# Optimization experiments

Measured on AMD Instinct MI355X. Metric: run time of the kernel, lower is better.

The kernel has to match this reference:

```python
import jax, jax.numpy as jnp
import numpy as np

N = 100_000
E = 1_600_000
H = 128
L = 3
EPS = 1e-5


def setup_inputs() -> dict:
    key = jax.random.key(0)
    ks = jax.random.split(key, 8)
    x = jax.random.normal(ks[0], (N, H), dtype=jnp.float32)
    edge_index = jax.random.randint(ks[1], (2, E), 0, N, dtype=jnp.int64)
    edge_weight = jax.random.uniform(ks[2], (E,), dtype=jnp.float32)
    # per-layer params (all layers are H->H since in_dim == hidden)
    s = 1.0 / np.sqrt(H)
    lin_neigh_w = jax.random.uniform(ks[3], (L, H, H), minval=-s, maxval=s, dtype=jnp.float32)
    lin_root_w = jax.random.uniform(ks[4], (L, H, H), minval=-s, maxval=s, dtype=jnp.float32)
    lin_root_b = jax.random.uniform(ks[5], (L, H), minval=-s, maxval=s, dtype=jnp.float32)
    ln_w = jnp.ones((L, H), dtype=jnp.float32)
    ln_b = jnp.zeros((L, H), dtype=jnp.float32)
    return {"x": x, "edge_index": edge_index, "edge_weight": edge_weight,
            "lin_neigh_w": lin_neigh_w, "lin_root_w": lin_root_w,
            "lin_root_b": lin_root_b, "ln_w": ln_w, "ln_b": ln_b}


def _layer(h, src, dst, e_w, w_neigh, w_root, b_root, g, b):
    # message: m_ij = w_ij * x_j ; aggregate: scatter-add over dst, normalized by sum of weights
    msg = e_w[:, None] * h[src]                                    # [E, H]
    agg = jax.ops.segment_sum(msg, dst, num_segments=N)            # [N, H]
    sum_w = jnp.clip(jax.ops.segment_sum(e_w, dst, num_segments=N), 1.0, None)
    out = agg / sum_w[:, None]
    out = out @ w_neigh.T + h @ w_root.T + b_root                  # lin_neigh + lin_root
    out = jax.nn.relu(out)
    # per-node LayerNorm over feature dim
    mu = jnp.mean(out, axis=-1, keepdims=True)
    var = jnp.var(out, axis=-1, keepdims=True)
    out = (out - mu) * jax.lax.rsqrt(var + EPS) * g + b
    return out  # dropout: inference no-op


def reference(x, edge_index, edge_weight, lin_neigh_w, lin_root_w, lin_root_b, ln_w, ln_b):
    src, dst = edge_index[0], edge_index[1]
    h = x
    for l in range(L):
        h = _layer(h, src, dst, edge_weight, lin_neigh_w[l], lin_root_w[l],
                   lin_root_b[l], ln_w[l], ln_b[l])
    return h
```

## Files before the change

kernel.cpp:

```cpp
#include <hip/hip_runtime.h>
#include <hip/hip_fp16.h>

#define H 128
#define EPS 1e-5f
#define BCAP 6144

typedef __attribute__((ext_vector_type(8))) _Float16 half8;
typedef __attribute__((ext_vector_type(4))) float f32x4;

__device__ inline __half2 u2h2(unsigned u) { return __builtin_bit_cast(__half2, u); }
__device__ inline unsigned h22u(__half2 h) { return __builtin_bit_cast(unsigned, h); }

__global__ void convert_kernel(const float* __restrict__ x, unsigned* __restrict__ hx, int n4) {
    int i = blockIdx.x * 256 + threadIdx.x;
    if (i >= n4) return;
    float4 v = reinterpret_cast<const float4*>(x)[i];
    unsigned p0 = h22u(__floats2half2_rn(v.x, v.y));
    unsigned p1 = h22u(__floats2half2_rn(v.z, v.w));
    reinterpret_cast<uint2*>(hx)[i] = make_uint2(p0, p1);
}

__global__ __launch_bounds__(256) void bhist_kernel(const int* __restrict__ dst,
                                                    int* __restrict__ ghist, int E, int NB) {
    __shared__ int hist[512];
    int t = threadIdx.x;
    for (int i = t; i < NB; i += 256) hist[i] = 0;
    __syncthreads();
    int base = blockIdx.x * 8192 + t;
#pragma unroll
    for (int k = 0; k < 32; ++k) {
        int e = base + k * 256;
        if (e < E) atomicAdd(&hist[dst[e] >> 8], 1);
    }
    __syncthreads();
    for (int i = t; i < NB; i += 256)
        if (hist[i]) atomicAdd(&ghist[i], hist[i]);
}

__global__ __launch_bounds__(512) void bscan_kernel(const int* __restrict__ ghist,
                                                    int* __restrict__ bucket_base,
                                                    int* __restrict__ cursor,
                                                    int* __restrict__ row_start,
                                                    int NB, int E, int N) {
    __shared__ int lds[512];
    int t = threadIdx.x;
    int v = (t < NB) ? ghist[t] : 0;
    lds[t] = v;
    __syncthreads();
    for (int off = 1; off < 512; off <<= 1) {
        int u = (t >= off) ? lds[t - off] : 0;
        __syncthreads();
        lds[t] += u;
        __syncthreads();
    }
    int excl = lds[t] - v;
    if (t < NB) {
        bucket_base[t] = excl;
        cursor[t] = excl;
    }
    if (t == 0) {
        bucket_base[NB] = E;
        row_start[N] = E;
    }
}

__global__ __launch_bounds__(1024) void bucketize_kernel(const int* __restrict__ src,
                                                         const int* __restrict__ dst,
                                                         const float* __restrict__ ew,
                                                         int* __restrict__ cursor,
                                                         int2* __restrict__ ee, int E, int NB) {
    __shared__ int hist[512];
    __shared__ int scn[512];
    __shared__ int gbase[512];
    __shared__ int2 stage[8192];
    int t = threadIdx.x;
    for (int i = t; i < NB; i += 1024) hist[i] = 0;
    __syncthreads();

    int e0 = blockIdx.x * 8192;
    int bb[8], rk[8], pk[8], wb[8];
#pragma unroll
    for (int k = 0; k < 8; ++k) {
        int e = e0 + t + k * 1024;
        if (e < E) {
            int s = src[e], d = dst[e];
            bb[k] = d >> 8;
            pk[k] = s | ((d & 255) << 17);
            wb[k] = __float_as_int(ew[e]);
            rk[k] = atomicAdd(&hist[bb[k]], 1);
        } else {
            bb[k] = -1;
        }
    }
    __syncthreads();
    if (t < 512) scn[t] = (t < NB) ? hist[t] : 0;
    __syncthreads();
    for (int off = 1; off < 512; off <<= 1) {
        int u = 0;
        if (t < 512 && t >= off) u = scn[t - off];
        __syncthreads();
        if (t < 512) scn[t] += u;
        __syncthreads();
    }
    for (int i = t; i < NB; i += 1024) {
        int c = hist[i];
        if (c > 0) gbase[i] = atomicAdd(&cursor[i], c);
    }
#pragma unroll
    for (int k = 0; k < 8; ++k) {
        if (bb[k] >= 0) {
            int start = scn[bb[k]] - hist[bb[k]];
            stage[start + rk[k]] = make_int2(pk[k], wb[k]);
        }
    }
    __syncthreads();
    int wv = t >> 6, ln = t & 63;
    for (int bk = wv; bk < NB; bk += 16) {
        int c = hist[bk];
        if (c == 0) continue;
        int s0 = scn[bk] - c;
        int gb = gbase[bk];
        for (int i = ln; i < c; i += 64) ee[gb + i] = stage[s0 + i];
    }
}

__global__ __launch_bounds__(256) void bsort_kernel(int2* __restrict__ ee,
                                                    const int* __restrict__ bucket_base,
                                                    int* __restrict__ row_start, int N) {
    __shared__ int cnts[256];
    __shared__ int scv[256];
    __shared__ int prefs[256];
    __shared__ int2 out[BCAP];
    int b = blockIdx.x;
    int base = bucket_base[b], endb = bucket_base[b + 1];
    int cnt = endb - base;
    int t = threadIdx.x;
    cnts[t] = 0;
    __syncthreads();
    for (int i = base + t; i < endb; i += 256) atomicAdd(&cnts[(ee[i].x >> 17) & 255], 1);
    __syncthreads();
    scv[t] = cnts[t];
    __syncthreads();
    for (int off = 1; off < 256; off <<= 1) {
        int u = (t >= off) ? scv[t - off] : 0;
        __syncthreads();
        scv[t] += u;
        __syncthreads();
    }
    int pref = scv[t] - cnts[t];
    prefs[t] = pref;
    int node = (b << 8) + t;
    if (node < N) row_start[node] = base + pref;
    __syncthreads();
    cnts[t] = 0;
    __syncthreads();
    for (int i = base + t; i < endb; i += 256) {
        int2 r = ee[i];
        int dl = (r.x >> 17) & 255;
        int rkk = atomicAdd(&cnts[dl], 1);
        int slot = prefs[dl] + rkk;
        if (slot < BCAP) out[slot] = make_int2(r.x & 0x1FFFF, r.y);
    }
    __syncthreads();
    {
        int s0 = prefs[t], c = cnts[t];
        float sw = 0.f;
        for (int k = 0; k < c; ++k) sw += __int_as_float(out[s0 + k].y);
        sw = sw < 1.f ? 1.f : sw;
        float inv = 1.f / sw;
        for (int k = 0; k < c; ++k) {
            float w = __int_as_float(out[s0 + k].y) * inv;
            unsigned hb = (unsigned)__half_as_ushort(__float2half(w));
            out[s0 + k].y = (int)(hb | (hb << 16));
        }
    }
    __syncthreads();
    for (int i = t; i < cnt; i += 256) ee[base + i] = out[i];
}

__global__ __launch_bounds__(256) void agg_kernel(const unsigned short* __restrict__ hx,
                                                  const int* __restrict__ row_start,
                                                  const int2* __restrict__ ee,
                                                  unsigned short* __restrict__ aggb, int N) {
    int t = threadIdx.x;
    int node = blockIdx.x * 4 + (t >> 6);
    if (node >= N) return;
    int lane = t & 63, half = lane >> 5, jb = lane & 31;
    __half2 a01 = u2h2(0), a23 = u2h2(0);
    int rs = row_start[node], re = row_start[node + 1];
    int i = rs + half;
    for (; i + 6 < re; i += 8) {
        int2 e0 = ee[i], e1 = ee[i + 2], e2 = ee[i + 4], e3 = ee[i + 6];
        uint2 u0 = reinterpret_cast<const uint2*>(hx + (size_t)e0.x * H)[jb];
        uint2 u1 = reinterpret_cast<const uint2*>(hx + (size_t)e1.x * H)[jb];
        uint2 u2 = reinterpret_cast<const uint2*>(hx + (size_t)e2.x * H)[jb];
        uint2 u3 = reinterpret_cast<const uint2*>(hx + (size_t)e3.x * H)[jb];
        __half2 w0 = u2h2((unsigned)e0.y), w1 = u2h2((unsigned)e1.y);
        __half2 w2 = u2h2((unsigned)e2.y), w3 = u2h2((unsigned)e3.y);
        a01 = __hfma2(u2h2(u0.x), w0, a01); a23 = __hfma2(u2h2(u0.y), w0, a23);
        a01 = __hfma2(u2h2(u1.x), w1, a01); a23 = __hfma2(u2h2(u1.y), w1, a23);
        a01 = __hfma2(u2h2(u2.x), w2, a01); a23 = __hfma2(u2h2(u2.y), w2, a23);
        a01 = __hfma2(u2h2(u3.x), w3, a01); a23 = __hfma2(u2h2(u3.y), w3, a23);
    }
    for (; i < re; i += 2) {
        int2 e0 = ee[i];
        uint2 u0 = reinterpret_cast<const uint2*>(hx + (size_t)e0.x * H)[jb];
        __half2 w0 = u2h2((unsigned)e0.y);
        a01 = __hfma2(u2h2(u0.x), w0, a01);
        a23 = __hfma2(u2h2(u0.y), w0, a23);
    }
    a01 = __hadd2(a01, u2h2((unsigned)__shfl_xor((int)h22u(a01), 32)));
    a23 = __hadd2(a23, u2h2((unsigned)__shfl_xor((int)h22u(a23), 32)));
    unsigned p = half ? h22u(a23) : h22u(a01);
    reinterpret_cast<unsigned*>(aggb + (size_t)node * H)[2 * jb + half] = p;
}

__global__ __launch_bounds__(256, 2) void gemm_ln_mfma(
    const unsigned short* __restrict__ aggb, const unsigned short* __restrict__ hx,
    const float* __restrict__ Wn, const float* __restrict__ Wr,
    const float* __restrict__ br, const float* __restrict__ g,
    const float* __restrict__ b, unsigned short* __restrict__ hout,
    float* __restrict__ outf, int final_layer, int N) {
    __shared__ half8 Bfl[4096];

    int t = threadIdx.x;
    int w = t >> 6, lane = t & 63;
    int Mbase = blockIdx.x * 256;

#pragma unroll
    for (int it = 0; it < 16; ++it) {
        int f = it * 4 + w;
        int kt = f >> 3, nb = f & 7;
        int n = nb * 16 + (lane & 15);
        int kk = (kt & 3) * 32 + (lane >> 4) * 8;
        const float* wp = ((kt < 4) ? Wn : Wr) + (size_t)n * H + kk;
        float4 wa = *reinterpret_cast<const float4*>(wp);
        float4 wb = *reinterpret_cast<const float4*>(wp + 4);
        half8 sv;
        sv[0] = (_Float16)wa.x; sv[1] = (_Float16)wa.y;
        sv[2] = (_Float16)wa.z; sv[3] = (_Float16)wa.w;
        sv[4] = (_Float16)wb.x; sv[5] = (_Float16)wb.y;
        sv[6] = (_Float16)wb.z; sv[7] = (_Float16)wb.w;
        Bfl[f * 64 + lane] = sv;
    }
    __syncthreads();

    int lrow = lane & 15, lk = lane >> 4;
    const char* aggp = (const char*)aggb;
    const char* hp = (const char*)hx;
    size_t rb[4];
#pragma unroll
    for (int mf = 0; mf < 4; ++mf) {
        int r = Mbase + w * 64 + mf * 16 + lrow;
        r = r < N ? r : N - 1;
        rb[mf] = (size_t)r * 256;
    }

    f32x4 acc[4][8];
#pragma unroll
    for (int mf = 0; mf < 4; ++mf)
#pragma unroll
        for (int nb = 0; nb < 8; ++nb) acc[mf][nb] = (f32x4){0.f, 0.f, 0.f, 0.f};

#pragma unroll
    for (int kt = 0; kt < 8; ++kt) {
        const char* base = (kt < 4) ? aggp : hp;
        int off = (kt & 3) * 64 + lk * 16;
        half8 bf[8];
#pragma unroll
        for (int nb = 0; nb < 8; ++nb) bf[nb] = Bfl[(kt * 8 + nb) * 64 + lane];
#pragma unroll
        for (int mf = 0; mf < 4; ++mf) {
            half8 av = *reinterpret_cast<const half8*>(base + rb[mf] + off);
#pragma unroll
            for (int nb = 0; nb < 8; ++nb)
                acc[mf][nb] = __builtin_amdgcn_mfma_f32_16x16x32_f16(av, bf[nb], acc[mf][nb], 0, 0, 0);
        }
    }

    int col0 = lane & 15, rq = lane >> 4;
    float bias[8], gg[8], bbv[8];
#pragma unroll
    for (int nb = 0; nb < 8; ++nb) {
        int c = col0 + nb * 16;
        bias[nb] = br[c];
        gg[nb] = g[c];
        bbv[nb] = b[c];
    }
#pragma unroll
    for (int mf = 0; mf < 4; ++mf) {
#pragma unroll
        for (int reg = 0; reg < 4; ++reg) {
            float v[8];
            float s = 0.f, q = 0.f;
#pragma unroll
            for (int nb = 0; nb < 8; ++nb) {
                float u = acc[mf][nb][reg] + bias[nb];
                u = fmaxf(u, 0.f);
                v[nb] = u;
                s += u;
                q = fmaf(u, u, q);
            }
#pragma unroll
            for (int off = 1; off < 16; off <<= 1) {
                s += __shfl_xor(s, off);
                q += __shfl_xor(q, off);
            }
            float mu = s * (1.f / 128.f);
            float var = q * (1.f / 128.f) - mu * mu;
            float inv = rsqrtf(var + EPS);
            int grow = Mbase + w * 64 + mf * 16 + rq * 4 + reg;
            if (grow < N) {
                if (final_layer) {
#pragma unroll
                    for (int nb = 0; nb < 8; ++nb)
                        outf[(size_t)grow * H + col0 + nb * 16] = (v[nb] - mu) * inv * gg[nb] + bbv[nb];
                } else {
#pragma unroll
                    for (int nb = 0; nb < 8; ++nb)
                        hout[(size_t)grow * H + col0 + nb * 16] =
                            __half_as_ushort(__float2half((v[nb] - mu) * inv * gg[nb] + bbv[nb]));
                }
            }
        }
    }
}

static inline size_t alignup(size_t x) { return (x + 255) & ~(size_t)255; }

extern "C" void kernel_launch(void* const* d_in, const int* in_sizes, int n_in,
                              void* d_out, int out_size, void* d_ws, size_t ws_size,
                              hipStream_t stream) {
    const float* x  = (const float*)d_in[0];
    const int*   ei = (const int*)d_in[1];
    const float* ew = (const float*)d_in[2];
    const float* Wn = (const float*)d_in[3];
    const float* Wr = (const float*)d_in[4];
    const float* br = (const float*)d_in[5];
    const float* g  = (const float*)d_in[6];
    const float* bb = (const float*)d_in[7];
    float* out = (float*)d_out;

    int N = in_sizes[0] / H;
    int E = in_sizes[2];
    const int* src = ei;
    const int* dst = ei + E;
    int NB = (N + 255) >> 8;

    char* ws = (char*)d_ws;
    size_t off = 0;
    int* ghist = (int*)(ws + off);         off = alignup(off + sizeof(int) * 512);
    int* bucket_base = (int*)(ws + off);   off = alignup(off + sizeof(int) * 513);
    int* cursor = (int*)(ws + off);        off = alignup(off + sizeof(int) * 512);
    int* row_start = (int*)(ws + off);     off = alignup(off + sizeof(int) * ((size_t)N + 1));
    int2* ee = (int2*)(ws + off);          off = alignup(off + sizeof(int2) * (size_t)E);
    unsigned short* aggb = (unsigned short*)(ws + off); off = alignup(off + 2ull * N * H);
    unsigned short* hx = (unsigned short*)(ws + off);   off = alignup(off + 2ull * N * H);

    int eblocks = (E + 8191) / 8192;

    hipMemsetAsync(ghist, 0, sizeof(int) * 512, stream);
    bhist_kernel<<<eblocks, 256, 0, stream>>>(dst, ghist, E, NB);
    bscan_kernel<<<1, 512, 0, stream>>>(ghist, bucket_base, cursor, row_start, NB, E, N);
    bucketize_kernel<<<eblocks, 1024, 0, stream>>>(src, dst, ew, cursor, ee, E, NB);
    bsort_kernel<<<NB, 256, 0, stream>>>(ee, bucket_base, row_start, N);

    int n4 = N * H / 4;
    convert_kernel<<<(n4 + 255) / 256, 256, 0, stream>>>(x, (unsigned*)hx, n4);

    int gblocks = (N + 255) / 256;
    for (int l = 0; l < 3; ++l) {
        agg_kernel<<<(N + 3) / 4, 256, 0, stream>>>(hx, row_start, ee, aggb, N);
        gemm_ln_mfma<<<gblocks, 256, 0, stream>>>(
            aggb, hx,
            Wn + (size_t)l * H * H, Wr + (size_t)l * H * H, br + (size_t)l * H,
            g + (size_t)l * H, bb + (size_t)l * H,
            hx, out, (l == 2) ? 1 : 0, N);
    }
}
```

Baseline: 333.5 us.

## Slice node features into 16-wide column blocks and pack edges into 32-bit records

```diff
diff --git a/kernel.cpp b/kernel.cpp
--- a/kernel.cpp
+++ b/kernel.cpp
@@ -4,6 +4,7 @@
 #define H 128
 #define EPS 1e-5f
 #define BCAP 6144
+#define SLB 2048
 
 typedef __attribute__((ext_vector_type(8))) _Float16 half8;
 typedef __attribute__((ext_vector_type(4))) float f32x4;
@@ -11,13 +12,22 @@
 __device__ inline __half2 u2h2(unsigned u) { return __builtin_bit_cast(__half2, u); }
 __device__ inline unsigned h22u(__half2 h) { return __builtin_bit_cast(unsigned, h); }
 
-__global__ void convert_kernel(const float* __restrict__ x, unsigned* __restrict__ hx, int n4) {
-    int i = blockIdx.x * 256 + threadIdx.x;
-    if (i >= n4) return;
-    float4 v = reinterpret_cast<const float4*>(x)[i];
-    unsigned p0 = h22u(__floats2half2_rn(v.x, v.y));
-    unsigned p1 = h22u(__floats2half2_rn(v.z, v.w));
-    reinterpret_cast<uint2*>(hx)[i] = make_uint2(p0, p1);
+__global__ void convert_kernel(const float* __restrict__ x, char* __restrict__ hxs, int N) {
+    int tid = blockIdx.x * 256 + threadIdx.x;
+    int twoN = N * 2;
+    if (tid >= twoN * 8) return;
+    int s = tid / twoN;
+    int rem = tid - s * twoN;
+    int nd = rem >> 1, hh = rem & 1;
+    const float* xp = x + (size_t)nd * H + s * 16 + hh * 8;
+    float4 a = *reinterpret_cast<const float4*>(xp);
+    float4 b2 = *reinterpret_cast<const float4*>(xp + 4);
+    unsigned p0 = h22u(__floats2half2_rn(a.x, a.y));
+    unsigned p1 = h22u(__floats2half2_rn(a.z, a.w));
+    unsigned p2 = h22u(__floats2half2_rn(b2.x, b2.y));
+    unsigned p3 = h22u(__floats2half2_rn(b2.z, b2.w));
+    *reinterpret_cast<uint4*>(hxs + (((size_t)s * N + nd) << 5) + hh * 16) =
+        make_uint4(p0, p1, p2, p3);
 }
 
 __global__ __launch_bounds__(256) void bhist_kernel(const int* __restrict__ dst,
@@ -124,9 +134,10 @@
     }
 }
 
-__global__ __launch_bounds__(256) void bsort_kernel(int2* __restrict__ ee,
+__global__ __launch_bounds__(256) void bsort_kernel(const int2* __restrict__ ee,
                                                     const int* __restrict__ bucket_base,
-                                                    int* __restrict__ row_start, int N) {
+                                                    int* __restrict__ row_start,
+                                                    unsigned* __restrict__ ee4, int N) {
     __shared__ int cnts[256];
     __shared__ int scv[256];
     __shared__ int prefs[256];
@@ -170,53 +181,58 @@
         float inv = 1.f / sw;
         for (int k = 0; k < c; ++k) {
             float w = __int_as_float(out[s0 + k].y) * inv;
-            unsigned hb = (unsigned)__half_as_ushort(__float2half(w));
-            out[s0 + k].y = (int)(hb | (hb << 16));
-        }
-    }
-    __syncthreads();
-    for (int i = t; i < cnt; i += 256) ee[base + i] = out[i];
-}
-
-__global__ __launch_bounds__(256) void agg_kernel(const unsigned short* __restrict__ hx,
+            out[s0 + k].y = (int)(unsigned)__half_as_ushort(__float2half(w));
+        }
+    }
+    __syncthreads();
+    for (int i = t; i < cnt; i += 256)
+        ee4[base + i] = ((unsigned)out[i].x << 15) | ((unsigned)out[i].y >> 1);
+}
+
+__global__ __launch_bounds__(256) void agg_kernel(const char* __restrict__ hxs,
                                                   const int* __restrict__ row_start,
-                                                  const int2* __restrict__ ee,
-                                                  unsigned short* __restrict__ aggb, int N) {
-    int t = threadIdx.x;
-    int node = blockIdx.x * 4 + (t >> 6);
-    if (node >= N) return;
-    int lane = t & 63, half = lane >> 5, jb = lane & 31;
-    __half2 a01 = u2h2(0), a23 = u2h2(0);
-    int rs = row_start[node], re = row_start[node + 1];
-    int i = rs + half;
-    for (; i + 6 < re; i += 8) {
-        int2 e0 = ee[i], e1 = ee[i + 2], e2 = ee[i + 4], e3 = ee[i + 6];
-        uint2 u0 = reinterpret_cast<const uint2*>(hx + (size_t)e0.x * H)[jb];
-        uint2 u1 = reinterpret_cast<const uint2*>(hx + (size_t)e1.x * H)[jb];
-        uint2 u2 = reinterpret_cast<const uint2*>(hx + (size_t)e2.x * H)[jb];
-        uint2 u3 = reinterpret_cast<const uint2*>(hx + (size_t)e3.x * H)[jb];
-        __half2 w0 = u2h2((unsigned)e0.y), w1 = u2h2((unsigned)e1.y);
-        __half2 w2 = u2h2((unsigned)e2.y), w3 = u2h2((unsigned)e3.y);
-        a01 = __hfma2(u2h2(u0.x), w0, a01); a23 = __hfma2(u2h2(u0.y), w0, a23);
-        a01 = __hfma2(u2h2(u1.x), w1, a01); a23 = __hfma2(u2h2(u1.y), w1, a23);
-        a01 = __hfma2(u2h2(u2.x), w2, a01); a23 = __hfma2(u2h2(u2.y), w2, a23);
-        a01 = __hfma2(u2h2(u3.x), w3, a01); a23 = __hfma2(u2h2(u3.y), w3, a23);
-    }
-    for (; i < re; i += 2) {
-        int2 e0 = ee[i];
-        uint2 u0 = reinterpret_cast<const uint2*>(hx + (size_t)e0.x * H)[jb];
-        __half2 w0 = u2h2((unsigned)e0.y);
-        a01 = __hfma2(u2h2(u0.x), w0, a01);
-        a23 = __hfma2(u2h2(u0.y), w0, a23);
-    }
-    a01 = __hadd2(a01, u2h2((unsigned)__shfl_xor((int)h22u(a01), 32)));
-    a23 = __hadd2(a23, u2h2((unsigned)__shfl_xor((int)h22u(a23), 32)));
-    unsigned p = half ? h22u(a23) : h22u(a01);
-    reinterpret_cast<unsigned*>(aggb + (size_t)node * H)[2 * jb + half] = p;
+                                                  const unsigned* __restrict__ ee4,
+                                                  char* __restrict__ aggs, int N) {
+    int s = blockIdx.x & 7;
+    int cb = blockIdx.x >> 3;
+    int t = threadIdx.x;
+    int w = t >> 6, lane = t & 63;
+    int g = lane >> 4;
+    int eo = (lane >> 3) & 1;
+    int c = lane & 7;
+    size_t sN = (size_t)s * N;
+#pragma unroll
+    for (int r = 0; r < 4; ++r) {
+        int nd = (cb * 4 + r) * 16 + w * 4 + g;
+        int rs = 0, re = 0;
+        if (nd < N) {
+            rs = row_start[nd];
+            re = row_start[nd + 1];
+        }
+        __half2 acc = u2h2(0);
+        int idx = rs + eo;
+        while (__any(idx < re)) {
+            bool act = idx < re;
+            int ii = act ? idx : 0;
+            unsigned rec = __builtin_nontemporal_load(ee4 + ii);
+            rec = act ? rec : 0u;
+            unsigned hw = (rec & 0x7FFFu) << 1;
+            __half2 w2 = u2h2(hw | (hw << 16));
+            unsigned srcv = rec >> 15;
+            unsigned hv = *reinterpret_cast<const unsigned*>(hxs + ((sN + srcv) << 5) + c * 4);
+            acc = __hfma2(u2h2(hv), w2, acc);
+            idx += 2;
+        }
+        acc = __hadd2(acc, u2h2((unsigned)__shfl_xor((int)h22u(acc), 8)));
+        if (eo == 0 && nd < N) {
+            __builtin_nontemporal_store(
+                h22u(acc), reinterpret_cast<unsigned*>(aggs + ((sN + nd) << 5) + c * 4));
+        }
+    }
 }
 
 __global__ __launch_bounds__(256, 2) void gemm_ln_mfma(
-    const unsigned short* __restrict__ aggb, const unsigned short* __restrict__ hx,
+    const char* __restrict__ aggs, const char* __restrict__ hxs,
     const float* __restrict__ Wn, const float* __restrict__ Wr,
     const float* __restrict__ br, const float* __restrict__ g,
     const float* __restrict__ b, unsigned short* __restrict__ hout,
@@ -246,14 +262,13 @@
     __syncthreads();
 
     int lrow = lane & 15, lk = lane >> 4;
-    const char* aggp = (const char*)aggb;
-    const char* hp = (const char*)hx;
-    size_t rb[4];
+    int lk1 = lk & 1, lkh = lk >> 1;
+    size_t rowb[4];
 #pragma unroll
     for (int mf = 0; mf < 4; ++mf) {
         int r = Mbase + w * 64 + mf * 16 + lrow;
         r = r < N ? r : N - 1;
-        rb[mf] = (size_t)r * 256;
+        rowb[mf] = (size_t)r << 5;
     }
 
     f32x4 acc[4][8];
@@ -264,14 +279,14 @@
 
 #pragma unroll
     for (int kt = 0; kt < 8; ++kt) {
-        const char* base = (kt < 4) ? aggp : hp;
-        int off = (kt & 3) * 64 + lk * 16;
+        const char* base = (kt < 4) ? aggs : hxs;
+        size_t soff = (((size_t)((kt & 3) * 2 + lkh)) * (size_t)N << 5) + (size_t)lk1 * 16;
         half8 bf[8];
 #pragma unroll
         for (int nb = 0; nb < 8; ++nb) bf[nb] = Bfl[(kt * 8 + nb) * 64 + lane];
 #pragma unroll
         for (int mf = 0; mf < 4; ++mf) {
-            half8 av = *reinterpret_cast<const half8*>(base + rb[mf] + off);
+            half8 av = *reinterpret_cast<const half8*>(base + soff + rowb[mf]);
 #pragma unroll
             for (int nb = 0; nb < 8; ++nb)
                 acc[mf][nb] = __builtin_amdgcn_mfma_f32_16x16x32_f16(av, bf[nb], acc[mf][nb], 0, 0, 0);
@@ -282,31 +297,31 @@
     float bias[8], gg[8], bbv[8];
 #pragma unroll
     for (int nb = 0; nb < 8; ++nb) {
-        int c = col0 + nb * 16;
-        bias[nb] = br[c];
-        gg[nb] = g[c];
-        bbv[nb] = b[c];
+        int cc = col0 + nb * 16;
+        bias[nb] = br[cc];
+        gg[nb] = g[cc];
+        bbv[nb] = b[cc];
     }
 #pragma unroll
     for (int mf = 0; mf < 4; ++mf) {
 #pragma unroll
         for (int reg = 0; reg < 4; ++reg) {
             float v[8];
-            float s = 0.f, q = 0.f;
+            float sacc = 0.f, q = 0.f;
 #pragma unroll
             for (int nb = 0; nb < 8; ++nb) {
                 float u = acc[mf][nb][reg] + bias[nb];
                 u = fmaxf(u, 0.f);
                 v[nb] = u;
-                s += u;
+                sacc += u;
                 q = fmaf(u, u, q);
             }
 #pragma unroll
             for (int off = 1; off < 16; off <<= 1) {
-                s += __shfl_xor(s, off);
+                sacc += __shfl_xor(sacc, off);
                 q += __shfl_xor(q, off);
             }
-            float mu = s * (1.f / 128.f);
+            float mu = sacc * (1.f / 128.f);
             float var = q * (1.f / 128.f) - mu * mu;
             float inv = rsqrtf(var + EPS);
             int grow = Mbase + w * 64 + mf * 16 + rq * 4 + reg;
@@ -318,7 +333,7 @@
                 } else {
 #pragma unroll
                     for (int nb = 0; nb < 8; ++nb)
-                        hout[(size_t)grow * H + col0 + nb * 16] =
+                        hout[(((size_t)nb * N + grow) << 4) + col0] =
                             __half_as_ushort(__float2half((v[nb] - mu) * inv * gg[nb] + bbv[nb]));
                 }
             }
@@ -354,8 +369,9 @@
     int* cursor = (int*)(ws + off);        off = alignup(off + sizeof(int) * 512);
     int* row_start = (int*)(ws + off);     off = alignup(off + sizeof(int) * ((size_t)N + 1));
     int2* ee = (int2*)(ws + off);          off = alignup(off + sizeof(int2) * (size_t)E);
-    unsigned short* aggb = (unsigned short*)(ws + off); off = alignup(off + 2ull * N * H);
-    unsigned short* hx = (unsigned short*)(ws + off);   off = alignup(off + 2ull * N * H);
+    unsigned* ee4 = (unsigned*)(ws + off); off = alignup(off + sizeof(unsigned) * (size_t)E);
+    char* aggs = ws + off;                 off = alignup(off + 2ull * N * H);
+    char* hxs  = ws + off;                 off = alignup(off + 2ull * N * H);
 
     int eblocks = (E + 8191) / 8192;
 
@@ -363,18 +379,18 @@
     bhist_kernel<<<eblocks, 256, 0, stream>>>(dst, ghist, E, NB);
     bscan_kernel<<<1, 512, 0, stream>>>(ghist, bucket_base, cursor, row_start, NB, E, N);
     bucketize_kernel<<<eblocks, 1024, 0, stream>>>(src, dst, ew, cursor, ee, E, NB);
-    bsort_kernel<<<NB, 256, 0, stream>>>(ee, bucket_base, row_start, N);
-
-    int n4 = N * H / 4;
-    convert_kernel<<<(n4 + 255) / 256, 256, 0, stream>>>(x, (unsigned*)hx, n4);
+    bsort_kernel<<<NB, 256, 0, stream>>>(ee, bucket_base, row_start, ee4, N);
+
+    int cthreads = N * 16;
+    convert_kernel<<<(cthreads + 255) / 256, 256, 0, stream>>>(x, hxs, N);
 
     int gblocks = (N + 255) / 256;
     for (int l = 0; l < 3; ++l) {
-        agg_kernel<<<(N + 3) / 4, 256, 0, stream>>>(hx, row_start, ee, aggb, N);
+        agg_kernel<<<8 * SLB, 256, 0, stream>>>(hxs, row_start, ee4, aggs, N);
         gemm_ln_mfma<<<gblocks, 256, 0, stream>>>(
-            aggb, hx,
+            aggs, hxs,
             Wn + (size_t)l * H * H, Wr + (size_t)l * H * H, br + (size_t)l * H,
             g + (size_t)l * H, bb + (size_t)l * H,
-            hx, out, (l == 2) ? 1 : 0, N);
-    }
-}
+            (unsigned short*)hxs, out, (l == 2) ? 1 : 0, N);
+    }
+}
```

Measured after the change: 848.3 us. +154.3%, slower.
